# Optimization experiments

Hardware: AMD Instinct MI355X
Metric: run time of the kernel (lower is better)

The kernel has to match this reference:

```python
import jax, jax.numpy as jnp
import numpy as np

S, B, DM, H, DFF = 2048, 4, 1024, 16, 4096
DK = DM // H  # 64, dv == dk
EPS = 1e-5

def layer_norm(x, g, b):
    mu = jnp.mean(x, axis=-1, keepdims=True)
    var = jnp.var(x, axis=-1, keepdims=True)
    return (x - mu) * jax.lax.rsqrt(var + EPS) * g + b

def setup_inputs() -> dict:
    key = jax.random.key(0)
    ks = jax.random.split(key, 12)
    sc = 0.02
    return {
        "X": jax.random.normal(ks[0], (S, B, DM), dtype=jnp.float32),
        # stacked per-head projections: weight [H, dk, dm], bias [H, dk]
        "WQ_w": jax.random.normal(ks[1], (H, DK, DM), dtype=jnp.float32) * sc,
        "WQ_b": jnp.zeros((H, DK), dtype=jnp.float32),
        "WK_w": jax.random.normal(ks[2], (H, DK, DM), dtype=jnp.float32) * sc,
        "WK_b": jnp.zeros((H, DK), dtype=jnp.float32),
        "WV_w": jax.random.normal(ks[3], (H, DK, DM), dtype=jnp.float32) * sc,
        "WV_b": jnp.zeros((H, DK), dtype=jnp.float32),
        "WO_w": jax.random.normal(ks[4], (DM, H * DK), dtype=jnp.float32) * sc,
        "WO_b": jnp.zeros((DM,), dtype=jnp.float32),
        "ln1_g": jnp.ones((DM,), dtype=jnp.float32),
        "ln1_b": jnp.zeros((DM,), dtype=jnp.float32),
        "W1": jax.random.normal(ks[5], (DFF, DM), dtype=jnp.float32) * sc,
        "b1": jnp.zeros((DFF,), dtype=jnp.float32),
        "W2": jax.random.normal(ks[6], (DM, DFF), dtype=jnp.float32) * sc,
        "b2": jnp.zeros((DM,), dtype=jnp.float32),
        "ln2_g": jnp.ones((DM,), dtype=jnp.float32),
        "ln2_b": jnp.zeros((DM,), dtype=jnp.float32),
    }

def reference(X, WQ_w, WQ_b, WK_w, WK_b, WV_w, WV_b, WO_w, WO_b,
              ln1_g, ln1_b, W1, b1, W2, b2, ln2_g, ln2_b):
    # --- self-attention (encoder: no causal mask, no key_mask, drop=0) ---
    # X: [S, B, DM]; per-head Q/K/V: [S, B, H, DK]
    Q = jnp.einsum('sbd,hkd->sbhk', X, WQ_w) + WQ_b
    K = jnp.einsum('sbd,hkd->sbhk', X, WK_w) + WK_b
    V = jnp.einsum('sbd,hvd->sbhv', X, WV_w) + WV_b
    scores = jnp.einsum('sbhk,lbhk->sbhl', Q, K) / jnp.sqrt(jnp.float32(DK))
    attn = jax.nn.softmax(scores, axis=-1)  # softmax over keys l
    ctx = jnp.einsum('sbhl,lbhv->sbhv', attn, V)
    # concat heads (head-major order matches torch.concat over head list)
    ctx = ctx.reshape(S, B, H * DK)
    y = ctx @ WO_w.T + WO_b
    X1 = layer_norm(y + X, ln1_g, ln1_b)
    # --- MLP (1 hidden layer, ReLU) ---
    h = jax.nn.relu(X1 @ W1.T + b1)
    m = h @ W2.T + b2
    return layer_norm(m + X1, ln2_g, ln2_b)
```

## Files before the change

### kernel.cpp

```cpp
#include <hip/hip_runtime.h>
#include <stdint.h>

typedef short bf16x8 __attribute__((ext_vector_type(8)));
typedef float f32x4 __attribute__((ext_vector_type(4)));
typedef float f32x16 __attribute__((ext_vector_type(16)));

__device__ __forceinline__ float bf2f(uint16_t u) {
    union { uint32_t i; float f; } c; c.i = ((uint32_t)u) << 16; return c.f;
}
__device__ __forceinline__ uint16_t f2bf(float f) {
    union { float f; uint32_t i; } c; c.f = f;
    uint32_t x = c.i;
    return (uint16_t)((x + 0x7fffu + ((x >> 16) & 1u)) >> 16);
}
__device__ __forceinline__ uint32_t pack2t(float lo, float hi) {
    union { float f; uint32_t u; } a, b;
    a.f = lo; b.f = hi;
    return __builtin_amdgcn_perm(b.u, a.u, 0x07060302u);
}

__device__ __forceinline__ float exp2r(float x) {
#if __has_builtin(__builtin_amdgcn_exp2f)
    return __builtin_amdgcn_exp2f(x);
#else
    return exp2f(x);
#endif
}

__device__ __forceinline__ void plane32_swap(uint32_t& a, uint32_t& b) {
#if __has_builtin(__builtin_amdgcn_permlane32_swap)
    typedef unsigned int u32x2 __attribute__((ext_vector_type(2)));
    u32x2 r = __builtin_amdgcn_permlane32_swap(a, b, false, false);
    a = r[0]; b = r[1];
#else
    asm volatile("v_permlane32_swap_b32 %0, %1" : "+v"(a), "+v"(b));
#endif
}

__device__ __forceinline__ void load_lds16(const void* g, void* lds) {
    using gp_t = const __attribute__((address_space(1))) uint32_t*;
    using lp_t = __attribute__((address_space(3))) uint32_t*;
    __builtin_amdgcn_global_load_lds(
        reinterpret_cast<gp_t>(reinterpret_cast<uintptr_t>(g)),
        reinterpret_cast<lp_t>((uint32_t)reinterpret_cast<uintptr_t>(lds)),
        16, 0, 0);
}

__global__ __launch_bounds__(256) void cvt_all(
    const float* __restrict__ X,
    const float* __restrict__ wqf, const float* __restrict__ wkf,
    const float* __restrict__ wvf, const float* __restrict__ wof,
    const float* __restrict__ w1f, const float* __restrict__ w2f,
    const float* __restrict__ bqf, const float* __restrict__ bkf,
    const float* __restrict__ bvf, const float* __restrict__ bof,
    const float* __restrict__ b1f, const float* __restrict__ b2f,
    uint16_t* __restrict__ Xb, uint16_t* __restrict__ wd, uint16_t* __restrict__ bd)
{
    const int b = blockIdx.x, tid = threadIdx.x;
    const size_t M = 1048576ull;
    const float* s; uint16_t* d; size_t i, off;
    if (b < 8192) {
        i = ((size_t)b * 256 + tid) * 4;
        s = X; off = i; d = Xb;
    } else if (b < 20480) {
        i = ((size_t)(b - 8192) * 256 + tid) * 4;
        d = wd;
        if (i < M)           { s = wqf; off = i; }
        else if (i < 2 * M)  { s = wkf; off = i - M; }
        else if (i < 3 * M)  { s = wvf; off = i - 2 * M; }
        else if (i < 4 * M)  { s = wof; off = i - 3 * M; }
        else if (i < 8 * M)  { s = w1f; off = i - 4 * M; }
        else                 { s = w2f; off = i - 8 * M; }
    } else {
        int j = tid * 4;
        d = bd;
        for (int p = 0; p < 9; ++p, j += 1024) {
            const float* sb; int ob;
            if (j < 1024)      { sb = bqf; ob = j; }
            else if (j < 2048) { sb = bkf; ob = j - 1024; }
            else if (j < 3072) { sb = bvf; ob = j - 2048; }
            else if (j < 4096) { sb = bof; ob = j - 3072; }
            else if (j < 8192) { sb = b1f; ob = j - 4096; }
            else               { sb = b2f; ob = j - 8192; }
            float4 x = *(const float4*)(sb + ob);
            ushort4 u;
            u.x = f2bf(x.x); u.y = f2bf(x.y); u.z = f2bf(x.z); u.w = f2bf(x.w);
            *(ushort4*)(d + j) = u;
        }
        return;
    }
    float4 x = *(const float4*)(s + off);
    ushort4 u;
    u.x = f2bf(x.x); u.y = f2bf(x.y); u.z = f2bf(x.z); u.w = f2bf(x.w);
    *(ushort4*)(d + i) = u;
}

template<int MODE, int NT>
__global__ __launch_bounds__(256) void gemm_bt(
    const uint16_t* __restrict__ A, const uint16_t* __restrict__ B,
    const uint16_t* __restrict__ bias, uint16_t* __restrict__ C,
    int K, int N, int relu)
{
    const int CT = NT / 32;
    __shared__ uint16_t sA[128 * 64];
    __shared__ uint16_t sB[NT * 64];
    const int tid = threadIdx.x;
    const int w = tid >> 6, ln = tid & 63;
    const int m = ln & 15, q = ln >> 4;
    const int wr = w >> 1, wc = w & 1;
    const int tm = blockIdx.y * 128, tn = blockIdx.x * NT;

    f32x4 zero = {0.f, 0.f, 0.f, 0.f};
    f32x4 acc[4][CT];
#pragma unroll
    for (int i = 0; i < 4; ++i)
#pragma unroll
        for (int j = 0; j < CT; ++j) acc[i][j] = zero;

    const int sr = tid >> 3;
    const int sc_ = tid & 7;
    const int g = sc_ ^ (sr & 7);

    for (int k0 = 0; k0 < K; k0 += 64) {
        __syncthreads();
#pragma unroll
        for (int i = 0; i < 4; ++i) {
            int r = i * 32 + sr;
            load_lds16(A + (size_t)(tm + r) * K + k0 + g * 8, &sA[(i * 32 + w * 8) * 64]);
        }
#pragma unroll
        for (int i = 0; i < NT / 32; ++i) {
            int r = i * 32 + sr;
            load_lds16(B + (size_t)(tn + r) * K + k0 + g * 8, &sB[(i * 32 + w * 8) * 64]);
        }
        __syncthreads();
#pragma unroll
        for (int kk = 0; kk < 2; ++kk) {
            bf16x8 af[4], bfr[CT];
            const int s = (kk * 4 + q) ^ (m & 7);
#pragma unroll
            for (int rt = 0; rt < 4; ++rt) {
                int R = wr * 64 + rt * 16 + m;
                af[rt] = *(const bf16x8*)&sA[R * 64 + s * 8];
            }
#pragma unroll
            for (int ct = 0; ct < CT; ++ct) {
                int R = wc * (NT / 2) + ct * 16 + m;
                bfr[ct] = *(const bf16x8*)&sB[R * 64 + s * 8];
            }
#pragma unroll
            for (int rt = 0; rt < 4; ++rt)
#pragma unroll
                for (int ct = 0; ct < CT; ++ct)
                    acc[rt][ct] = __builtin_amdgcn_mfma_f32_16x16x32_bf16(
                        af[rt], bfr[ct], acc[rt][ct], 0, 0, 0);
        }
    }

    const int sect = tn >> 10;
#pragma unroll
    for (int ct = 0; ct < CT; ++ct) {
        int col = tn + wc * (NT / 2) + ct * 16 + m;
        float bv = bf2f(bias[col]);
#pragma unroll
        for (int rt = 0; rt < 4; ++rt) {
            int rowb = tm + wr * 64 + rt * 16 + q * 4;
#pragma unroll
            for (int rg = 0; rg < 4; ++rg) {
                int t = rowb + rg;
                float v = acc[rt][ct][rg] + bv;
                if (relu) v = fmaxf(v, 0.f);
                size_t off;
                if (MODE == 0) {
                    off = (size_t)t * N + col;
                } else {
                    int c = col & 1023;
                    int bh = (t & 3) * 16 + (c >> 6);
                    if (sect == 0) {
                        off = (size_t)bh * 131072 + (t >> 2) * 64 + (c & 63);
                        v *= 0.18033688f;
                    } else if (sect == 1) {
                        off = 8388608ull + (size_t)bh * 131072 + (t >> 2) * 64 + (c & 63);
                    } else {
                        off = 16777216ull + (size_t)bh * 131072 + (size_t)(c & 63) * 2048 + (t >> 2);
                    }
                }
                C[off] = f2bf(v);
            }
        }
    }
}

__global__ __launch_bounds__(256) void attn2(
    const uint16_t* __restrict__ Qh, const uint16_t* __restrict__ Kh,
    const uint16_t* __restrict__ Vt, uint16_t* __restrict__ CTX)
{
    __shared__ uint16_t sK[2][64 * 64];
    __shared__ uint16_t sV[2][64 * 64];

    const int tid = threadIdx.x;
    const int w = tid >> 6, ln = tid & 63;
    const int m5 = ln & 31, h5 = ln >> 5;
    const int bh = blockIdx.x, qt = blockIdx.y;
    const uint16_t* Qb = Qh + (size_t)bh * 131072;
    const uint16_t* Kb = Kh + (size_t)bh * 131072;
    const uint16_t* Vb = Vt + (size_t)bh * 131072;

    const int qrow = qt * 128 + w * 32 + m5;
    bf16x8 qf[4];
#pragma unroll
    for (int ks = 0; ks < 4; ++ks)
        qf[ks] = *(const bf16x8*)(Qb + (size_t)qrow * 64 + ks * 16 + h5 * 8);

    f32x16 Oa[2];
#pragma unroll
    for (int nb = 0; nb < 2; ++nb)
#pragma unroll
        for (int i = 0; i < 16; ++i) Oa[nb][i] = 0.f;
    float psum = 0.f;

    const int sr = tid >> 3;
    const int g = (tid & 7) ^ (sr & 7);

    {
        load_lds16(Kb + (size_t)sr * 64 + g * 8,            &sK[0][tid * 8]);
        load_lds16(Kb + (size_t)(sr + 32) * 64 + g * 8,     &sK[0][2048 + tid * 8]);
        load_lds16(Vb + (size_t)sr * 2048 + g * 8,          &sV[0][tid * 8]);
        load_lds16(Vb + (size_t)(sr + 32) * 2048 + g * 8,   &sV[0][2048 + tid * 8]);
    }

    for (int c = 0; c < 32; ++c) {
        const int cur = c & 1;
        __syncthreads();
        if (c + 1 < 32) {
            const int nc = c + 1;
            uint16_t* kd = &sK[cur ^ 1][0];
            uint16_t* vd = &sV[cur ^ 1][0];
            load_lds16(Kb + (size_t)(nc * 64 + sr) * 64 + g * 8,        kd + tid * 8);
            load_lds16(Kb + (size_t)(nc * 64 + sr + 32) * 64 + g * 8,   kd + 2048 + tid * 8);
            load_lds16(Vb + (size_t)sr * 2048 + nc * 64 + g * 8,        vd + tid * 8);
            load_lds16(Vb + (size_t)(sr + 32) * 2048 + nc * 64 + g * 8, vd + 2048 + tid * 8);
        }

        bf16x8 pf[4];
#pragma unroll
        for (int kb = 0; kb < 2; ++kb) {
            f32x16 acc;
#pragma unroll
            for (int i = 0; i < 16; ++i) acc[i] = 0.f;
#pragma unroll
            for (int ks = 0; ks < 4; ++ks) {
                int row = kb * 32 + m5;
                int ph = (2 * ks + h5) ^ (m5 & 7);
                bf16x8 kf = *(const bf16x8*)&sK[cur][row * 64 + ph * 8];
                acc = __builtin_amdgcn_mfma_f32_32x32x16_bf16(kf, qf[ks], acc, 0, 0, 0);
            }
#pragma unroll
            for (int ksl = 0; ksl < 2; ++ksl) {
                float p0 = exp2r(acc[8 * ksl + 0]);
                float p1 = exp2r(acc[8 * ksl + 1]);
                float p2 = exp2r(acc[8 * ksl + 2]);
                float p3 = exp2r(acc[8 * ksl + 3]);
                float p4 = exp2r(acc[8 * ksl + 4]);
                float p5 = exp2r(acc[8 * ksl + 5]);
                float p6 = exp2r(acc[8 * ksl + 6]);
                float p7 = exp2r(acc[8 * ksl + 7]);
                psum += ((p0 + p1) + (p2 + p3)) + ((p4 + p5) + (p6 + p7));
                uint32_t x0 = pack2t(p0, p1);
                uint32_t x1 = pack2t(p2, p3);
                uint32_t y0 = pack2t(p4, p5);
                uint32_t y1 = pack2t(p6, p7);
                plane32_swap(x0, y0);
                plane32_swap(x1, y1);
                union { uint32_t u[4]; bf16x8 v; } pu;
                pu.u[0] = x0; pu.u[1] = x1; pu.u[2] = y0; pu.u[3] = y1;
                pf[kb * 2 + ksl] = pu.v;
            }
        }

#pragma unroll
        for (int ks = 0; ks < 4; ++ks) {
#pragma unroll
            for (int nb = 0; nb < 2; ++nb) {
                int vrow = nb * 32 + m5;
                int ph = (2 * ks + h5) ^ (m5 & 7);
                bf16x8 vf = *(const bf16x8*)&sV[cur][vrow * 64 + ph * 8];
                Oa[nb] = __builtin_amdgcn_mfma_f32_32x32x16_bf16(pf[ks], vf, Oa[nb], 0, 0, 0);
            }
        }
    }

    float l = psum + __shfl_xor(psum, 32);
    float linv = 1.f / l;
    float li[16];
#pragma unroll
    for (int a = 0; a < 4; ++a)
#pragma unroll
        for (int r = 0; r < 4; ++r)
            li[4 * a + r] = __shfl(linv, r + 8 * a + 4 * h5);

    const int b_ = bh >> 4, h_ = bh & 15;
#pragma unroll
    for (int nb = 0; nb < 2; ++nb)
#pragma unroll
        for (int a = 0; a < 4; ++a)
#pragma unroll
            for (int r = 0; r < 4; ++r) {
                int qr = r + 8 * a + 4 * h5;
                int s = qt * 128 + w * 32 + qr;
                int col = h_ * 64 + nb * 32 + m5;
                CTX[(size_t)(s * 4 + b_) * 1024 + col] = f2bf(Oa[nb][4 * a + r] * li[4 * a + r]);
            }
}

template<bool RES_F32, bool OUT_F32>
__global__ __launch_bounds__(256) void ln_resid(
    const uint16_t* __restrict__ Y, const void* __restrict__ Xp,
    const float* __restrict__ G, const float* __restrict__ Bv,
    void* __restrict__ Op)
{
    const int row = blockIdx.x, tid = threadIdx.x;
    const size_t base = (size_t)row * 1024 + tid * 4;
    ushort4 yv = *(const ushort4*)(Y + base);
    float x0, x1, x2, x3;
    if (RES_F32) {
        float4 xv = *(const float4*)((const float*)Xp + base);
        x0 = xv.x; x1 = xv.y; x2 = xv.z; x3 = xv.w;
    } else {
        ushort4 xv = *(const ushort4*)((const uint16_t*)Xp + base);
        x0 = bf2f(xv.x); x1 = bf2f(xv.y); x2 = bf2f(xv.z); x3 = bf2f(xv.w);
    }
    float v0 = bf2f(yv.x) + x0;
    float v1 = bf2f(yv.y) + x1;
    float v2 = bf2f(yv.z) + x2;
    float v3 = bf2f(yv.w) + x3;
    float s = v0 + v1 + v2 + v3;
    float ss = v0 * v0 + v1 * v1 + v2 * v2 + v3 * v3;
#pragma unroll
    for (int off = 32; off > 0; off >>= 1) {
        s += __shfl_down(s, off);
        ss += __shfl_down(ss, off);
    }
    __shared__ float rs[4], rss[4];
    if ((tid & 63) == 0) { rs[tid >> 6] = s; rss[tid >> 6] = ss; }
    __syncthreads();
    float S = rs[0] + rs[1] + rs[2] + rs[3];
    float SS = rss[0] + rss[1] + rss[2] + rss[3];
    const float invn = 1.f / 1024.f;
    float mu = S * invn;
    float var = SS * invn - mu * mu;
    float rstd = rsqrtf(var + 1e-5f);
    float4 gv = *(const float4*)(G + tid * 4);
    float4 bv = *(const float4*)(Bv + tid * 4);
    float o0 = (v0 - mu) * rstd * gv.x + bv.x;
    float o1 = (v1 - mu) * rstd * gv.y + bv.y;
    float o2 = (v2 - mu) * rstd * gv.z + bv.z;
    float o3 = (v3 - mu) * rstd * gv.w + bv.w;
    if (OUT_F32) {
        float4 o = {o0, o1, o2, o3};
        *(float4*)((float*)Op + base) = o;
    } else {
        ushort4 o;
        o.x = f2bf(o0); o.y = f2bf(o1); o.z = f2bf(o2); o.w = f2bf(o3);
        *(ushort4*)((uint16_t*)Op + base) = o;
    }
}

extern "C" void kernel_launch(void* const* d_in, const int* in_sizes, int n_in,
                              void* d_out, int out_size, void* d_ws, size_t ws_size,
                              hipStream_t stream)
{
    const float* X    = (const float*)d_in[0];
    const float* WQw  = (const float*)d_in[1];
    const float* WQb  = (const float*)d_in[2];
    const float* WKw  = (const float*)d_in[3];
    const float* WKb  = (const float*)d_in[4];
    const float* WVw  = (const float*)d_in[5];
    const float* WVb  = (const float*)d_in[6];
    const float* WOw  = (const float*)d_in[7];
    const float* WOb  = (const float*)d_in[8];
    const float* ln1g = (const float*)d_in[9];
    const float* ln1b = (const float*)d_in[10];
    const float* W1   = (const float*)d_in[11];
    const float* b1   = (const float*)d_in[12];
    const float* W2   = (const float*)d_in[13];
    const float* b2   = (const float*)d_in[14];
    const float* ln2g = (const float*)d_in[15];
    const float* ln2b = (const float*)d_in[16];

    uint16_t* ws = (uint16_t*)d_ws;
    const size_t E = 8192ull * 1024ull;
    const size_t MW = 1048576ull;
    uint16_t* Xb   = ws;
    uint16_t* qh   = ws + E;
    uint16_t* kh   = ws + 2 * E;
    uint16_t* vt   = ws + 3 * E;
    uint16_t* ctx  = ws + 4 * E;
    uint16_t* y    = qh;
    uint16_t* x1   = kh;
    uint16_t* m2   = vt;
    uint16_t* hbuf = ws + 5 * E;
    uint16_t* wq   = ws + 9 * E;
    uint16_t* wo   = wq + 3 * MW;
    uint16_t* w1   = wo + MW;
    uint16_t* w2   = w1 + 4 * MW;
    uint16_t* bq   = w2 + 4 * MW;
    uint16_t* bo   = bq + 3072;
    uint16_t* bb1  = bo + 1024;
    uint16_t* bb2  = bb1 + 4096;

    cvt_all<<<dim3(20481), dim3(256), 0, stream>>>(
        X, WQw, WKw, WVw, WOw, W1, W2, WQb, WKb, WVb, WOb, b1, b2,
        Xb, wq, bq);

    dim3 blk(256);
    gemm_bt<3, 128><<<dim3(24, 64), blk, 0, stream>>>(Xb,   wq, bq,  qh,   1024, 3072, 0);
    attn2<<<dim3(64, 16), blk, 0, stream>>>(qh, kh, vt, ctx);
    gemm_bt<0, 64><<<dim3(16, 64),  blk, 0, stream>>>(ctx,  wo, bo,  y,    1024, 1024, 0);
    ln_resid<true, false><<<dim3(8192), blk, 0, stream>>>(y, X, ln1g, ln1b, x1);
    gemm_bt<0, 128><<<dim3(32, 64), blk, 0, stream>>>(x1,   w1, bb1, hbuf, 1024, 4096, 1);
    gemm_bt<0, 64><<<dim3(16, 64),  blk, 0, stream>>>(hbuf, w2, bb2, m2,   4096, 1024, 0);
    ln_resid<false, true><<<dim3(8192), blk, 0, stream>>>(m2, x1, ln2g, ln2b, d_out);
}
```

Before: 543.8 us.

## Add 256x256-tile 8-wave GEMM with ping-pong LDS pipelining for QKV and FFN1

Introduces a new GEMM kernel using 512-thread blocks, 256x256 output tiles, double-buffered direct-to-LDS loads with XOR swizzle, XCD-aware block remapping, and interleaved prefetch/MFMA phases with setprio. It replaces the QKV projection and the first FFN GEMM, which were using the smaller-tile kernel. The aim is more data reuse per tile and overlap of global loads with MFMA work. The cost is 128KB of dynamic LDS per block, heavy register pressure, and fewer blocks per CU. The old kernel's MODE 3 path is reduced to row-major stores only, since MODE 3 now goes through the new kernel.

```diff
diff --git a/kernel.cpp b/kernel.cpp
--- a/kernel.cpp
+++ b/kernel.cpp
@@ -157,7 +157,6 @@
         }
     }
 
-    const int sect = tn >> 10;
 #pragma unroll
     for (int ct = 0; ct < CT; ++ct) {
         int col = tn + wc * (NT / 2) + ct * 16 + m;
@@ -169,6 +168,167 @@
             for (int rg = 0; rg < 4; ++rg) {
                 int t = rowb + rg;
                 float v = acc[rt][ct][rg] + bv;
+                if (relu) v = fmaxf(v, 0.f);
+                C[(size_t)t * N + col] = f2bf(v);
+            }
+        }
+    }
+}
+
+template<int MODE>
+__global__ __launch_bounds__(512, 2) void gemm8(
+    const uint16_t* __restrict__ A, const uint16_t* __restrict__ B,
+    const uint16_t* __restrict__ bias, uint16_t* __restrict__ C,
+    int K, int N, int NBX, int relu)
+{
+    extern __shared__ uint16_t smem[];
+
+    const int tid = threadIdx.x;
+    const int w = tid >> 6, ln = tid & 63;
+    const int m = ln & 15, q = ln >> 4;
+    const int wr = w >> 2, wc = w & 3;
+
+    const int nwg = gridDim.x;
+    const int bid = blockIdx.x;
+    const int wg = (bid & 7) * (nwg >> 3) + (bid >> 3);
+    const int bx = wg % NBX, by = wg / NBX;
+    const int tm = by * 256, tn = bx * 256;
+
+    const int sr = tid >> 3;
+    const int g = (tid & 7) ^ (sr & 7);
+    const int wbase = w * 512;
+
+    const int KT = K >> 6;
+
+    f32x4 acc[8][4];
+#pragma unroll
+    for (int i = 0; i < 8; ++i)
+#pragma unroll
+        for (int j = 0; j < 4; ++j) acc[i][j] = f32x4{0.f, 0.f, 0.f, 0.f};
+
+    auto stage2 = [&](int buf, int t, int i0) {
+        uint16_t* dA = smem + buf * 16384;
+        uint16_t* dB = smem + 32768 + buf * 16384;
+#pragma unroll
+        for (int i = i0; i < i0 + 2; ++i) {
+            load_lds16(A + (size_t)(tm + i * 64 + sr) * K + t * 64 + g * 8,
+                       dA + i * 4096 + wbase);
+            load_lds16(B + (size_t)(tn + i * 64 + sr) * K + t * 64 + g * 8,
+                       dB + i * 4096 + wbase);
+        }
+    };
+
+    stage2(0, 0, 0);
+    stage2(0, 0, 2);
+    asm volatile("s_waitcnt vmcnt(0)" ::: "memory");
+    __builtin_amdgcn_s_barrier();
+
+    for (int t = 0; t < KT; ++t) {
+        const int cur = t & 1;
+        const uint16_t* pA = smem + cur * 16384;
+        const uint16_t* pB = smem + 32768 + cur * 16384;
+        const bool pf = (t + 1 < KT);
+
+        bf16x8 bfrag[4], afrag[4];
+
+        {
+            const int s = q ^ (m & 7);
+#pragma unroll
+            for (int nf = 0; nf < 4; ++nf)
+                bfrag[nf] = *(const bf16x8*)&pB[(wc * 64 + nf * 16 + m) * 64 + s * 8];
+#pragma unroll
+            for (int mf = 0; mf < 4; ++mf)
+                afrag[mf] = *(const bf16x8*)&pA[(wr * 128 + mf * 16 + m) * 64 + s * 8];
+        }
+        if (pf) stage2(cur ^ 1, t + 1, 0);
+        __builtin_amdgcn_s_barrier();
+        asm volatile("s_waitcnt lgkmcnt(0)" ::: "memory");
+        __builtin_amdgcn_sched_barrier(0);
+        __builtin_amdgcn_s_setprio(1);
+#pragma unroll
+        for (int mf = 0; mf < 4; ++mf)
+#pragma unroll
+            for (int nf = 0; nf < 4; ++nf)
+                acc[mf][nf] = __builtin_amdgcn_mfma_f32_16x16x32_bf16(
+                    afrag[mf], bfrag[nf], acc[mf][nf], 0, 0, 0);
+        __builtin_amdgcn_s_setprio(0);
+        __builtin_amdgcn_s_barrier();
+
+        {
+            const int s = q ^ (m & 7);
+#pragma unroll
+            for (int mf = 0; mf < 4; ++mf)
+                afrag[mf] = *(const bf16x8*)&pA[(wr * 128 + (mf + 4) * 16 + m) * 64 + s * 8];
+        }
+        if (pf) stage2(cur ^ 1, t + 1, 2);
+        __builtin_amdgcn_s_barrier();
+        asm volatile("s_waitcnt lgkmcnt(0)" ::: "memory");
+        __builtin_amdgcn_sched_barrier(0);
+        __builtin_amdgcn_s_setprio(1);
+#pragma unroll
+        for (int mf = 0; mf < 4; ++mf)
+#pragma unroll
+            for (int nf = 0; nf < 4; ++nf)
+                acc[mf + 4][nf] = __builtin_amdgcn_mfma_f32_16x16x32_bf16(
+                    afrag[mf], bfrag[nf], acc[mf + 4][nf], 0, 0, 0);
+        __builtin_amdgcn_s_setprio(0);
+        __builtin_amdgcn_s_barrier();
+
+        {
+            const int s = (4 + q) ^ (m & 7);
+#pragma unroll
+            for (int nf = 0; nf < 4; ++nf)
+                bfrag[nf] = *(const bf16x8*)&pB[(wc * 64 + nf * 16 + m) * 64 + s * 8];
+#pragma unroll
+            for (int mf = 0; mf < 4; ++mf)
+                afrag[mf] = *(const bf16x8*)&pA[(wr * 128 + mf * 16 + m) * 64 + s * 8];
+        }
+        __builtin_amdgcn_s_barrier();
+        asm volatile("s_waitcnt lgkmcnt(0)" ::: "memory");
+        __builtin_amdgcn_sched_barrier(0);
+        __builtin_amdgcn_s_setprio(1);
+#pragma unroll
+        for (int mf = 0; mf < 4; ++mf)
+#pragma unroll
+            for (int nf = 0; nf < 4; ++nf)
+                acc[mf][nf] = __builtin_amdgcn_mfma_f32_16x16x32_bf16(
+                    afrag[mf], bfrag[nf], acc[mf][nf], 0, 0, 0);
+        __builtin_amdgcn_s_setprio(0);
+        __builtin_amdgcn_s_barrier();
+
+        {
+            const int s = (4 + q) ^ (m & 7);
+#pragma unroll
+            for (int mf = 0; mf < 4; ++mf)
+                afrag[mf] = *(const bf16x8*)&pA[(wr * 128 + (mf + 4) * 16 + m) * 64 + s * 8];
+        }
+        __builtin_amdgcn_s_barrier();
+        asm volatile("s_waitcnt lgkmcnt(0)" ::: "memory");
+        __builtin_amdgcn_sched_barrier(0);
+        __builtin_amdgcn_s_setprio(1);
+#pragma unroll
+        for (int mf = 0; mf < 4; ++mf)
+#pragma unroll
+            for (int nf = 0; nf < 4; ++nf)
+                acc[mf + 4][nf] = __builtin_amdgcn_mfma_f32_16x16x32_bf16(
+                    afrag[mf], bfrag[nf], acc[mf + 4][nf], 0, 0, 0);
+        __builtin_amdgcn_s_setprio(0);
+        if (pf) asm volatile("s_waitcnt vmcnt(0)" ::: "memory");
+        __builtin_amdgcn_s_barrier();
+    }
+
+    const int sect = tn >> 10;
+#pragma unroll
+    for (int nf = 0; nf < 4; ++nf) {
+        int col = tn + wc * 64 + nf * 16 + m;
+        float bv = bf2f(bias[col]);
+#pragma unroll
+        for (int mf = 0; mf < 8; ++mf) {
+            int rowb = tm + wr * 128 + mf * 16 + q * 4;
+#pragma unroll
+            for (int rg = 0; rg < 4; ++rg) {
+                int t = rowb + rg;
+                float v = acc[mf][nf][rg] + bv;
                 if (relu) v = fmaxf(v, 0.f);
                 size_t off;
                 if (MODE == 0) {
@@ -409,16 +569,25 @@
     uint16_t* bb1  = bo + 1024;
     uint16_t* bb2  = bb1 + 4096;
 
+    static bool attr_set = false;
+    if (!attr_set) {
+        (void)hipFuncSetAttribute(reinterpret_cast<const void*>(gemm8<3>),
+                                  hipFuncAttributeMaxDynamicSharedMemorySize, 131072);
+        (void)hipFuncSetAttribute(reinterpret_cast<const void*>(gemm8<0>),
+                                  hipFuncAttributeMaxDynamicSharedMemorySize, 131072);
+        attr_set = true;
+    }
+
     cvt_all<<<dim3(20481), dim3(256), 0, stream>>>(
         X, WQw, WKw, WVw, WOw, W1, W2, WQb, WKb, WVb, WOb, b1, b2,
         Xb, wq, bq);
 
     dim3 blk(256);
-    gemm_bt<3, 128><<<dim3(24, 64), blk, 0, stream>>>(Xb,   wq, bq,  qh,   1024, 3072, 0);
+    gemm8<3><<<dim3(384), dim3(512), 131072, stream>>>(Xb, wq, bq, qh, 1024, 3072, 12, 0);
     attn2<<<dim3(64, 16), blk, 0, stream>>>(qh, kh, vt, ctx);
     gemm_bt<0, 64><<<dim3(16, 64),  blk, 0, stream>>>(ctx,  wo, bo,  y,    1024, 1024, 0);
     ln_resid<true, false><<<dim3(8192), blk, 0, stream>>>(y, X, ln1g, ln1b, x1);
-    gemm_bt<0, 128><<<dim3(32, 64), blk, 0, stream>>>(x1,   w1, bb1, hbuf, 1024, 4096, 1);
+    gemm8<0><<<dim3(512), dim3(512), 131072, stream>>>(x1, w1, bb1, hbuf, 1024, 4096, 16, 1);
     gemm_bt<0, 64><<<dim3(16, 64),  blk, 0, stream>>>(hbuf, w2, bb2, m2,   4096, 1024, 0);
     ln_resid<false, true><<<dim3(8192), blk, 0, stream>>>(m2, x1, ln2g, ln2b, d_out);
 }
```

After: 557.0 us. 2.4% more time.

## Swizzle W2 GEMM blocks per XCD and compute softmax row sums with MFMA

Applied to the files above, without the earlier changes.

Adds an optional XCD-aware block remapping to the GEMM and enables it for the down-projection (K=4096). The remap groups each XCD's blocks into contiguous row tiles so the A tiles are reused in that XCD's L2. Separately, the attention kernel drops the scalar row-sum adds and cross-lane shuffles for the softmax denominator. Instead it runs an extra MFMA of P against a ones vector, using the bf16-rounded P values, which adds matrix-core work per chunk.

```diff
diff --git a/kernel.cpp b/kernel.cpp
--- a/kernel.cpp
+++ b/kernel.cpp
@@ -95,11 +95,11 @@
     *(ushort4*)(d + i) = u;
 }
 
-template<int MODE, int NT>
+template<int MODE, int NT, int SWZ>
 __global__ __launch_bounds__(256) void gemm_bt(
     const uint16_t* __restrict__ A, const uint16_t* __restrict__ B,
     const uint16_t* __restrict__ bias, uint16_t* __restrict__ C,
-    int K, int N, int relu)
+    int K, int N, int nbx, int relu)
 {
     const int CT = NT / 32;
     __shared__ uint16_t sA[128 * 64];
@@ -108,7 +108,18 @@
     const int w = tid >> 6, ln = tid & 63;
     const int m = ln & 15, q = ln >> 4;
     const int wr = w >> 1, wc = w & 1;
-    const int tm = blockIdx.y * 128, tn = blockIdx.x * NT;
+
+    int bx, by;
+    if (SWZ) {
+        const int lin = blockIdx.x;
+        const int xcd = lin & 7, idx = lin >> 3;
+        const int per = (gridDim.x >> 3) / nbx;
+        by = xcd * per + idx / nbx;
+        bx = idx % nbx;
+    } else {
+        bx = blockIdx.x; by = blockIdx.y;
+    }
+    const int tm = by * 128, tn = bx * NT;
 
     f32x4 zero = {0.f, 0.f, 0.f, 0.f};
     f32x4 acc[4][CT];
@@ -212,12 +223,17 @@
     for (int ks = 0; ks < 4; ++ks)
         qf[ks] = *(const bf16x8*)(Qb + (size_t)qrow * 64 + ks * 16 + h5 * 8);
 
-    f32x16 Oa[2];
+    f32x16 Oa[2], Lacc;
 #pragma unroll
     for (int nb = 0; nb < 2; ++nb)
 #pragma unroll
         for (int i = 0; i < 16; ++i) Oa[nb][i] = 0.f;
-    float psum = 0.f;
+#pragma unroll
+    for (int i = 0; i < 16; ++i) Lacc[i] = 0.f;
+
+    union { uint16_t u[8]; bf16x8 v; } one8;
+#pragma unroll
+    for (int i = 0; i < 8; ++i) one8.u[i] = 0x3F80;
 
     const int sr = tid >> 3;
     const int g = (tid & 7) ^ (sr & 7);
@@ -265,7 +281,6 @@
                 float p5 = exp2r(acc[8 * ksl + 5]);
                 float p6 = exp2r(acc[8 * ksl + 6]);
                 float p7 = exp2r(acc[8 * ksl + 7]);
-                psum += ((p0 + p1) + (p2 + p3)) + ((p4 + p5) + (p6 + p7));
                 uint32_t x0 = pack2t(p0, p1);
                 uint32_t x1 = pack2t(p2, p3);
                 uint32_t y0 = pack2t(p4, p5);
@@ -280,6 +295,7 @@
 
 #pragma unroll
         for (int ks = 0; ks < 4; ++ks) {
+            Lacc = __builtin_amdgcn_mfma_f32_32x32x16_bf16(pf[ks], one8.v, Lacc, 0, 0, 0);
 #pragma unroll
             for (int nb = 0; nb < 2; ++nb) {
                 int vrow = nb * 32 + m5;
@@ -290,14 +306,9 @@
         }
     }
 
-    float l = psum + __shfl_xor(psum, 32);
-    float linv = 1.f / l;
-    float li[16];
-#pragma unroll
-    for (int a = 0; a < 4; ++a)
-#pragma unroll
-        for (int r = 0; r < 4; ++r)
-            li[4 * a + r] = __shfl(linv, r + 8 * a + 4 * h5);
+    float Li[16];
+#pragma unroll
+    for (int j = 0; j < 16; ++j) Li[j] = 1.f / Lacc[j];
 
     const int b_ = bh >> 4, h_ = bh & 15;
 #pragma unroll
@@ -309,7 +320,7 @@
                 int qr = r + 8 * a + 4 * h5;
                 int s = qt * 128 + w * 32 + qr;
                 int col = h_ * 64 + nb * 32 + m5;
-                CTX[(size_t)(s * 4 + b_) * 1024 + col] = f2bf(Oa[nb][4 * a + r] * li[4 * a + r]);
+                CTX[(size_t)(s * 4 + b_) * 1024 + col] = f2bf(Oa[nb][4 * a + r] * Li[4 * a + r]);
             }
 }
 
@@ -414,11 +425,11 @@
         Xb, wq, bq);
 
     dim3 blk(256);
-    gemm_bt<3, 128><<<dim3(24, 64), blk, 0, stream>>>(Xb,   wq, bq,  qh,   1024, 3072, 0);
+    gemm_bt<3, 128, 0><<<dim3(24, 64), blk, 0, stream>>>(Xb,   wq, bq,  qh,   1024, 3072, 0, 0);
     attn2<<<dim3(64, 16), blk, 0, stream>>>(qh, kh, vt, ctx);
-    gemm_bt<0, 64><<<dim3(16, 64),  blk, 0, stream>>>(ctx,  wo, bo,  y,    1024, 1024, 0);
+    gemm_bt<0, 64, 0><<<dim3(16, 64),  blk, 0, stream>>>(ctx,  wo, bo,  y,    1024, 1024, 0, 0);
     ln_resid<true, false><<<dim3(8192), blk, 0, stream>>>(y, X, ln1g, ln1b, x1);
-    gemm_bt<0, 128><<<dim3(32, 64), blk, 0, stream>>>(x1,   w1, bb1, hbuf, 1024, 4096, 1);
-    gemm_bt<0, 64><<<dim3(16, 64),  blk, 0, stream>>>(hbuf, w2, bb2, m2,   4096, 1024, 0);
+    gemm_bt<0, 128, 0><<<dim3(32, 64), blk, 0, stream>>>(x1,   w1, bb1, hbuf, 1024, 4096, 0, 1);
+    gemm_bt<0, 64, 1><<<dim3(1024), blk, 0, stream>>>(hbuf, w2, bb2, m2,   4096, 1024, 16, 0);
     ln_resid<false, true><<<dim3(8192), blk, 0, stream>>>(m2, x1, ln2g, ln2b, d_out);
 }
```

Result: slower. 559.3 us (+2.8%).
